# Optimization experiments

Hardware: AMD Instinct MI355X
Metric: run time of the kernel (lower is better)

The kernel has to match this reference:

```python
import jax, jax.numpy as jnp
import numpy as np

N_NODES = 100000
N_GRAPHS = 512
HID = 128
IN_DIM = 128
OUT_DIM = 10
N_EDGES = 1600000


def gcn_conv(x, src, dst, W, b, n):
    # PyG GCNConv: add self-loops, symmetric normalization D^-1/2 (A+I) D^-1/2, then linear.
    h = x @ W  # [N, H]
    deg = jnp.zeros((n,), h.dtype).at[dst].add(1.0) + 1.0  # +1 self-loop
    dinv = jax.lax.rsqrt(deg)
    norm = dinv[src] * dinv[dst]  # [E]
    agg = jnp.zeros_like(h).at[dst].add(h[src] * norm[:, None])
    agg = agg + h * (dinv * dinv)[:, None]  # self-loop messages
    return agg + b


def setup_inputs() -> dict:
    key = jax.random.key(0)
    ks = jax.random.split(key, 12)
    x = jax.random.normal(ks[0], (N_NODES, IN_DIM), jnp.float32)
    edge_index = jax.random.randint(ks[1], (2, N_EDGES), 0, N_NODES)
    batch = jnp.sort(jax.random.randint(ks[2], (N_NODES,), 0, N_GRAPHS))
    def lin(k, fan_in, shape):
        bound = 1.0 / np.sqrt(fan_in)
        return jax.random.uniform(k, shape, jnp.float32, -bound, bound)
    W1 = lin(ks[3], IN_DIM, (IN_DIM, HID)); b1 = lin(ks[4], IN_DIM, (HID,))
    W2 = lin(ks[5], HID, (HID, HID)); b2 = lin(ks[6], HID, (HID,))
    W3 = lin(ks[7], HID, (HID, HID)); b3 = lin(ks[8], HID, (HID,))
    Wc1 = lin(ks[9], 2 * HID, (2 * HID, HID)); bc1 = lin(ks[9], 2 * HID, (HID,))
    Wc2 = lin(ks[10], HID, (HID, OUT_DIM)); bc2 = lin(ks[11], HID, (OUT_DIM,))
    return {"x": x, "edge_index": edge_index, "batch": batch,
            "W1": W1, "b1": b1, "W2": W2, "b2": b2, "W3": W3, "b3": b3,
            "Wc1": Wc1, "bc1": bc1, "Wc2": Wc2, "bc2": bc2}


def reference(x, edge_index, batch, W1, b1, W2, b2, W3, b3, Wc1, bc1, Wc2, bc2):
    src, dst = edge_index[0], edge_index[1]
    n = x.shape[0]
    h = jax.nn.relu(gcn_conv(x, src, dst, W1, b1, n))
    h = jax.nn.relu(gcn_conv(h, src, dst, W2, b2, n))
    h = gcn_conv(h, src, dst, W3, b3, n)  # no relu after last conv
    # global mean pool
    sums = jax.ops.segment_sum(h, batch, num_segments=N_GRAPHS)
    cnt = jax.ops.segment_sum(jnp.ones((n,), h.dtype), batch, num_segments=N_GRAPHS)
    mean = sums / jnp.maximum(cnt, 1.0)[:, None]
    # global max pool
    mx = jax.ops.segment_max(h, batch, num_segments=N_GRAPHS)
    mx = jnp.where(jnp.isfinite(mx), mx, 0.0)
    g = jnp.concatenate([mean, mx], axis=1)  # [G, 2H]
    g = jax.nn.relu(g @ Wc1 + bc1)
    return g @ Wc2 + bc2
```

## Files before the change

### kernel.cpp

```cpp
#include <hip/hip_runtime.h>

#define H 128
#define CAP 64

typedef __attribute__((ext_vector_type(8))) short bf16x8;
typedef __attribute__((ext_vector_type(4))) float f32x4;

__device__ __forceinline__ unsigned short f2bf(float f) {
  unsigned u = __float_as_uint(f);
  unsigned r = u + 0x7FFFu + ((u >> 16) & 1u);
  return (unsigned short)(r >> 16);
}
__device__ __forceinline__ float bf2f(unsigned short s) {
  return __uint_as_float(((unsigned)s) << 16);
}

__global__ __launch_bounds__(256) void setup_all(
    const float* __restrict__ x,
    const float* __restrict__ W1, const float* __restrict__ W2, const float* __restrict__ W3,
    unsigned short* __restrict__ Xb, unsigned short* __restrict__ Wt,
    int* __restrict__ csr_src, int cap4,
    unsigned short* __restrict__ P, unsigned short* __restrict__ Q,
    int* __restrict__ cursor, int cur4,
    int n, int totalX4) {
  long long i = (long long)blockIdx.x * 256 + threadIdx.x;
  if (i < totalX4) {
    float4 v = *(const float4*)(x + i * 4);
    ushort4 o;
    o.x = f2bf(v.x); o.y = f2bf(v.y); o.z = f2bf(v.z); o.w = f2bf(v.w);
    *(ushort4*)(Xb + i * 4) = o;
    return;
  }
  i -= totalX4;
  if (i < cap4) {
    *(int4*)(csr_src + i * 4) = make_int4(n, n, n, n);
    return;
  }
  i -= cap4;
  if (i < 3 * H * H) {
    int w = (int)(i >> 14);
    int rem = (int)i & (H * H - 1);
    int c = rem >> 7;
    int k = rem & 127;
    const float* W = (w == 0) ? W1 : (w == 1) ? W2 : W3;
    Wt[i] = f2bf(W[(size_t)k * H + c]);
    return;
  }
  i -= 3 * H * H;
  if (i < cur4) {
    *(int4*)(cursor + i * 4) = make_int4(0, 0, 0, 0);
    return;
  }
  i -= cur4;
  if (i < H) {
    P[(size_t)n * H + i] = 0;
    Q[(size_t)n * H + i] = 0;
  }
}

__global__ __launch_bounds__(256) void csr_fill_fixed(
    const int* __restrict__ src, const int* __restrict__ dst,
    int* __restrict__ cursor, int* __restrict__ csr_src,
    int ne, int range, int slices) {
  int r = blockIdx.x & 7;
  int slice = blockIdx.x >> 3;
  int ne4 = ne / 4;
  int chunk4 = (ne4 + slices - 1) / slices;
  int beg4 = slice * chunk4;
  int end4 = beg4 + chunk4; if (end4 > ne4) end4 = ne4;
  int lo = r * range;
  int hi = lo + range;
  for (int e4 = beg4 + threadIdx.x; e4 < end4; e4 += 256) {
    int e = e4 * 4;
    int4 d = *(const int4*)(dst + e);
    if (d.x >= lo && d.x < hi) { int p = atomicAdd(&cursor[d.x], 1); if (p < CAP) csr_src[(size_t)d.x * CAP + p] = src[e + 0]; }
    if (d.y >= lo && d.y < hi) { int p = atomicAdd(&cursor[d.y], 1); if (p < CAP) csr_src[(size_t)d.y * CAP + p] = src[e + 1]; }
    if (d.z >= lo && d.z < hi) { int p = atomicAdd(&cursor[d.z], 1); if (p < CAP) csr_src[(size_t)d.z * CAP + p] = src[e + 2]; }
    if (d.w >= lo && d.w < hi) { int p = atomicAdd(&cursor[d.w], 1); if (p < CAP) csr_src[(size_t)d.w * CAP + p] = src[e + 3]; }
  }
  if (r == 0 && slice == 0) {
    int base = ne4 * 4;
    int t = base + threadIdx.x;
    if (t < ne) {
      int d = dst[t];
      int p = atomicAdd(&cursor[d], 1);
      if (p < CAP) csr_src[(size_t)d * CAP + p] = src[t];
    }
  }
}

__global__ void dinv_gstart(const int* __restrict__ deg, float* __restrict__ dinv,
                            const int* __restrict__ batch, int* __restrict__ g_start,
                            int n, int G) {
  int i = blockIdx.x * blockDim.x + threadIdx.x;
  if (i >= n) return;
  dinv[i] = rsqrtf((float)(deg[i] + 1));
  int b = batch[i];
  int prev = (i == 0) ? -1 : batch[i - 1];
  for (int g = prev + 1; g <= b; ++g) g_start[g] = i;
  if (i == n - 1) {
    for (int g = b + 1; g <= G; ++g) g_start[g] = n;
  }
}

#define SWLD 136
__global__ __launch_bounds__(256) void gemm_mfma(
    const unsigned short* __restrict__ Ab, const unsigned short* __restrict__ Wt,
    const float* __restrict__ dinv, unsigned short* __restrict__ outb, int n) {
  __shared__ unsigned short sW[H * SWLD];
  int tid = threadIdx.x;
  {
    int c = tid >> 1, hh = tid & 1;
    const int4* s = (const int4*)(Wt + (size_t)c * H + hh * 64);
    int4* d = (int4*)(sW + (size_t)c * SWLD + hh * 64);
#pragma unroll
    for (int i = 0; i < 8; ++i) d[i] = s[i];
  }
  __syncthreads();

  int wave = tid >> 6;
  int lane = tid & 63;
  int m = lane & 15;
  int quad = lane >> 4;
  int row = blockIdx.x * 64 + wave * 16 + m;
  bool rv = row < n;

  f32x4 acc[8];
#pragma unroll
  for (int t = 0; t < 8; ++t) acc[t] = (f32x4){0.f, 0.f, 0.f, 0.f};

  const unsigned short* arow = Ab + (size_t)(rv ? row : 0) * H;
#pragma unroll
  for (int k0 = 0; k0 < H; k0 += 32) {
    bf16x8 af;
    if (rv) af = *(const bf16x8*)(arow + k0 + quad * 8);
    else    af = (bf16x8){0, 0, 0, 0, 0, 0, 0, 0};
#pragma unroll
    for (int ct = 0; ct < 8; ++ct) {
      bf16x8 bfr = *(const bf16x8*)(sW + (size_t)(ct * 16 + m) * SWLD + k0 + quad * 8);
      acc[ct] = __builtin_amdgcn_mfma_f32_16x16x32_bf16(af, bfr, acc[ct], 0, 0, 0);
    }
  }

  int orow0 = blockIdx.x * 64 + wave * 16 + quad * 4;
#pragma unroll
  for (int r = 0; r < 4; ++r) {
    int orow = orow0 + r;
    if (orow < n) {
      float dv = dinv[orow];
      unsigned short* o = outb + (size_t)orow * H + m;
#pragma unroll
      for (int ct = 0; ct < 8; ++ct) o[ct * 16] = f2bf(acc[ct][r] * dv);
    }
  }
}

template <bool RELU, bool OUTF32>
__global__ __launch_bounds__(256) void aggregate_bf(
    const unsigned short* __restrict__ hs, const int* __restrict__ deg,
    const int* __restrict__ csr_src, const float* __restrict__ dinv,
    const float* __restrict__ b, void* __restrict__ outv, int n) {
  int node = blockIdx.x * 8 + (threadIdx.x >> 5);
  if (node >= n) return;
  int c = (threadIdx.x & 31) << 2;
  int beg = node * CAP;
  int end = beg + ((deg[node] + 7) & ~7);

  ushort4 sv = *(const ushort4*)(hs + (size_t)node * H + c);
  float4 acc;
  acc.x = bf2f(sv.x); acc.y = bf2f(sv.y); acc.z = bf2f(sv.z); acc.w = bf2f(sv.w);

  int4 ia, ib;
  if (beg < end) {
    ia = *(const int4*)(csr_src + beg);
    ib = *(const int4*)(csr_src + beg + 4);
  }
  for (int k = beg; k < end; k += 8) {
    int4 ca = ia, cb = ib;
    int kn = k + 8;
    if (kn < end) {
      ia = *(const int4*)(csr_src + kn);
      ib = *(const int4*)(csr_src + kn + 4);
    }
    ushort4 v0 = *(const ushort4*)(hs + (size_t)ca.x * H + c);
    ushort4 v1 = *(const ushort4*)(hs + (size_t)ca.y * H + c);
    ushort4 v2 = *(const ushort4*)(hs + (size_t)ca.z * H + c);
    ushort4 v3 = *(const ushort4*)(hs + (size_t)ca.w * H + c);
    ushort4 v4 = *(const ushort4*)(hs + (size_t)cb.x * H + c);
    ushort4 v5 = *(const ushort4*)(hs + (size_t)cb.y * H + c);
    ushort4 v6 = *(const ushort4*)(hs + (size_t)cb.z * H + c);
    ushort4 v7 = *(const ushort4*)(hs + (size_t)cb.w * H + c);
    acc.x += ((bf2f(v0.x) + bf2f(v1.x)) + (bf2f(v2.x) + bf2f(v3.x))) +
             ((bf2f(v4.x) + bf2f(v5.x)) + (bf2f(v6.x) + bf2f(v7.x)));
    acc.y += ((bf2f(v0.y) + bf2f(v1.y)) + (bf2f(v2.y) + bf2f(v3.y))) +
             ((bf2f(v4.y) + bf2f(v5.y)) + (bf2f(v6.y) + bf2f(v7.y)));
    acc.z += ((bf2f(v0.z) + bf2f(v1.z)) + (bf2f(v2.z) + bf2f(v3.z))) +
             ((bf2f(v4.z) + bf2f(v5.z)) + (bf2f(v6.z) + bf2f(v7.z)));
    acc.w += ((bf2f(v0.w) + bf2f(v1.w)) + (bf2f(v2.w) + bf2f(v3.w))) +
             ((bf2f(v4.w) + bf2f(v5.w)) + (bf2f(v6.w) + bf2f(v7.w)));
  }

  float dv = dinv[node];
  float4 bb = *(const float4*)(b + c);
  float4 o;
  o.x = fmaf(acc.x, dv, bb.x);
  o.y = fmaf(acc.y, dv, bb.y);
  o.z = fmaf(acc.z, dv, bb.z);
  o.w = fmaf(acc.w, dv, bb.w);
  if (RELU) {
    o.x = fmaxf(o.x, 0.f); o.y = fmaxf(o.y, 0.f);
    o.z = fmaxf(o.z, 0.f); o.w = fmaxf(o.w, 0.f);
  }
  if (OUTF32) {
    *(float4*)((float*)outv + (size_t)node * H + c) = o;
  } else {
    ushort4 ob;
    ob.x = f2bf(o.x); ob.y = f2bf(o.y); ob.z = f2bf(o.z); ob.w = f2bf(o.w);
    *(ushort4*)((unsigned short*)outv + (size_t)node * H + c) = ob;
  }
}

__global__ __launch_bounds__(256) void pool2(
    const float* __restrict__ h, const int* __restrict__ g_start,
    float* __restrict__ gmean, float* __restrict__ gmax, int n) {
  __shared__ float ssum[16][64];
  __shared__ float smax[16][64];
  int g = blockIdx.x >> 1;
  int half = blockIdx.x & 1;
  int beg = g_start[g];
  int end = g_start[g + 1];
  int q = threadIdx.x >> 4;
  int c = (threadIdx.x & 15) << 2;
  int cg = half * 64 + c;

  float4 s = make_float4(0.f, 0.f, 0.f, 0.f);
  float4 m = make_float4(-INFINITY, -INFINITY, -INFINITY, -INFINITY);
  for (int node = beg + q; node < end; node += 16) {
    float4 v = *(const float4*)(h + (size_t)node * H + cg);
    s.x += v.x; s.y += v.y; s.z += v.z; s.w += v.w;
    m.x = fmaxf(m.x, v.x); m.y = fmaxf(m.y, v.y);
    m.z = fmaxf(m.z, v.z); m.w = fmaxf(m.w, v.w);
  }
  *(float4*)&ssum[q][c] = s;
  *(float4*)&smax[q][c] = m;
  __syncthreads();

  int cnt = end - beg;
  int t = threadIdx.x;
  if (t < 64) {
    float tot = 0.f;
#pragma unroll
    for (int qq = 0; qq < 16; ++qq) tot += ssum[qq][t];
    gmean[(size_t)g * H + half * 64 + t] = tot / fmaxf((float)cnt, 1.0f);
  } else if (t < 128) {
    int cc = t - 64;
    float mx = -INFINITY;
#pragma unroll
    for (int qq = 0; qq < 16; ++qq) mx = fmaxf(mx, smax[qq][cc]);
    gmax[(size_t)g * H + half * 64 + cc] = (cnt == 0) ? 0.0f : mx;
  }
}

__global__ __launch_bounds__(128) void classify_kernel(
    const float* __restrict__ gmean, const float* __restrict__ gmax,
    const float* __restrict__ Wc1, const float* __restrict__ bc1,
    const float* __restrict__ Wc2, const float* __restrict__ bc2,
    float* __restrict__ out) {
  __shared__ float gv[2 * H];
  __shared__ float hid[H];
  int gid = blockIdx.x;
  int t = threadIdx.x;
  gv[t] = gmean[(size_t)gid * H + t];
  gv[H + t] = gmax[(size_t)gid * H + t];
  __syncthreads();
  float acc = 0.f;
#pragma unroll 8
  for (int k = 0; k < 2 * H; ++k) acc = fmaf(gv[k], Wc1[(size_t)k * H + t], acc);
  hid[t] = fmaxf(acc + bc1[t], 0.f);
  __syncthreads();
  if (t < 10) {
    float a2 = 0.f;
    for (int j = 0; j < H; ++j) a2 = fmaf(hid[j], Wc2[(size_t)j * 10 + t], a2);
    out[(size_t)gid * 10 + t] = a2 + bc2[t];
  }
}

extern "C" void kernel_launch(void* const* d_in, const int* in_sizes, int n_in,
                              void* d_out, int out_size, void* d_ws, size_t ws_size,
                              hipStream_t stream) {
  const float* x    = (const float*)d_in[0];
  const int* ei     = (const int*)d_in[1];
  const int* batch  = (const int*)d_in[2];
  const float* W1   = (const float*)d_in[3];
  const float* b1   = (const float*)d_in[4];
  const float* W2   = (const float*)d_in[5];
  const float* b2   = (const float*)d_in[6];
  const float* W3   = (const float*)d_in[7];
  const float* b3   = (const float*)d_in[8];
  const float* Wc1  = (const float*)d_in[9];
  const float* bc1  = (const float*)d_in[10];
  const float* Wc2  = (const float*)d_in[11];
  const float* bc2  = (const float*)d_in[12];
  float* out = (float*)d_out;

  const int n  = in_sizes[2];
  const int ne = in_sizes[1] / 2;
  const int G  = 512;
  const size_t NFb = (size_t)(n + 1) * H;

  const int* src = ei;
  const int* dst = ei + ne;

  unsigned short* P_bf = (unsigned short*)d_ws;
  unsigned short* Q_bf = P_bf + NFb;
  float*          F2f  = (float*)(Q_bf + NFb);
  unsigned short* Xb   = (unsigned short*)F2f;
  int* csr_src = (int*)(F2f + (size_t)n * H);
  const size_t csr_cap = (size_t)n * CAP;
  char* p = (char*)(csr_src + csr_cap);
  int*            cursor   = (int*)p;            p += (size_t)n * 4;
  float*          dinv     = (float*)p;          p += (size_t)n * 4;
  int*            g_start  = (int*)p;            p += (size_t)(G + 1) * 4;
  float*          gmean    = (float*)p;          p += (size_t)G * H * 4;
  float*          gmax     = (float*)p;          p += (size_t)G * H * 4;
  p = (char*)(((uintptr_t)p + 255) & ~(uintptr_t)255);
  unsigned short* Wt       = (unsigned short*)p; p += (size_t)3 * H * H * 2;

  {
    int totalX4 = n * H / 4;
    int cap4 = (int)(csr_cap / 4);
    int cur4 = n / 4;
    long long tot = (long long)totalX4 + cap4 + 3 * H * H + cur4 + H;
    int blocks = (int)((tot + 255) / 256);
    setup_all<<<blocks, 256, 0, stream>>>(x, W1, W2, W3, Xb, Wt, csr_src, cap4,
                                          P_bf, Q_bf, cursor, cur4, n, totalX4);
  }

  int range = (n + 7) / 8;
  csr_fill_fixed<<<128 * 8, 256, 0, stream>>>(src, dst, cursor, csr_src, ne, range, 128);
  dinv_gstart<<<(n + 255) / 256, 256, 0, stream>>>(cursor, dinv, batch, g_start, n, G);

  const int tile_grid = (n + 63) / 64;
  const int node_grid = (n + 7) / 8;

  gemm_mfma<<<tile_grid, 256, 0, stream>>>(Xb, Wt, dinv, Q_bf, n);
  aggregate_bf<true, false><<<node_grid, 256, 0, stream>>>(Q_bf, cursor, csr_src, dinv, b1, P_bf, n);

  gemm_mfma<<<tile_grid, 256, 0, stream>>>(P_bf, Wt + H * H, dinv, Q_bf, n);
  aggregate_bf<true, false><<<node_grid, 256, 0, stream>>>(Q_bf, cursor, csr_src, dinv, b2, P_bf, n);

  gemm_mfma<<<tile_grid, 256, 0, stream>>>(P_bf, Wt + 2 * H * H, dinv, Q_bf, n);
  aggregate_bf<false, true><<<node_grid, 256, 0, stream>>>(Q_bf, cursor, csr_src, dinv, b3, F2f, n);

  pool2<<<2 * G, 256, 0, stream>>>(F2f, g_start, gmean, gmax, n);
  classify_kernel<<<G, 128, 0, stream>>>(gmean, gmax, Wc1, bc1, Wc2, bc2, out);
}
```

Baseline: 460.7 us.

## Drop CSR sentinel padding fill and handle degree remainder with scalar tail loop

```diff
diff --git a/kernel.cpp b/kernel.cpp
--- a/kernel.cpp
+++ b/kernel.cpp
@@ -19,8 +19,6 @@
     const float* __restrict__ x,
     const float* __restrict__ W1, const float* __restrict__ W2, const float* __restrict__ W3,
     unsigned short* __restrict__ Xb, unsigned short* __restrict__ Wt,
-    int* __restrict__ csr_src, int cap4,
-    unsigned short* __restrict__ P, unsigned short* __restrict__ Q,
     int* __restrict__ cursor, int cur4,
     int n, int totalX4) {
   long long i = (long long)blockIdx.x * 256 + threadIdx.x;
@@ -32,11 +30,6 @@
     return;
   }
   i -= totalX4;
-  if (i < cap4) {
-    *(int4*)(csr_src + i * 4) = make_int4(n, n, n, n);
-    return;
-  }
-  i -= cap4;
   if (i < 3 * H * H) {
     int w = (int)(i >> 14);
     int rem = (int)i & (H * H - 1);
@@ -49,12 +42,6 @@
   i -= 3 * H * H;
   if (i < cur4) {
     *(int4*)(cursor + i * 4) = make_int4(0, 0, 0, 0);
-    return;
-  }
-  i -= cur4;
-  if (i < H) {
-    P[(size_t)n * H + i] = 0;
-    Q[(size_t)n * H + i] = 0;
   }
 }
 
@@ -163,25 +150,18 @@
   int node = blockIdx.x * 8 + (threadIdx.x >> 5);
   if (node >= n) return;
   int c = (threadIdx.x & 31) << 2;
-  int beg = node * CAP;
-  int end = beg + ((deg[node] + 7) & ~7);
+  int dg = deg[node];
+  int beg  = node * CAP;
+  int end8 = beg + (dg & ~7);
+  int end  = beg + dg;
 
   ushort4 sv = *(const ushort4*)(hs + (size_t)node * H + c);
   float4 acc;
   acc.x = bf2f(sv.x); acc.y = bf2f(sv.y); acc.z = bf2f(sv.z); acc.w = bf2f(sv.w);
 
-  int4 ia, ib;
-  if (beg < end) {
-    ia = *(const int4*)(csr_src + beg);
-    ib = *(const int4*)(csr_src + beg + 4);
-  }
-  for (int k = beg; k < end; k += 8) {
-    int4 ca = ia, cb = ib;
-    int kn = k + 8;
-    if (kn < end) {
-      ia = *(const int4*)(csr_src + kn);
-      ib = *(const int4*)(csr_src + kn + 4);
-    }
+  for (int k = beg; k < end8; k += 8) {
+    int4 ca = *(const int4*)(csr_src + k);
+    int4 cb = *(const int4*)(csr_src + k + 4);
     ushort4 v0 = *(const ushort4*)(hs + (size_t)ca.x * H + c);
     ushort4 v1 = *(const ushort4*)(hs + (size_t)ca.y * H + c);
     ushort4 v2 = *(const ushort4*)(hs + (size_t)ca.z * H + c);
@@ -198,6 +178,12 @@
              ((bf2f(v4.z) + bf2f(v5.z)) + (bf2f(v6.z) + bf2f(v7.z)));
     acc.w += ((bf2f(v0.w) + bf2f(v1.w)) + (bf2f(v2.w) + bf2f(v3.w))) +
              ((bf2f(v4.w) + bf2f(v5.w)) + (bf2f(v6.w) + bf2f(v7.w)));
+  }
+  for (int k = end8; k < end; ++k) {
+    int s = csr_src[k];
+    ushort4 v = *(const ushort4*)(hs + (size_t)s * H + c);
+    acc.x += bf2f(v.x); acc.y += bf2f(v.y);
+    acc.z += bf2f(v.z); acc.w += bf2f(v.w);
   }
 
   float dv = dinv[node];
@@ -306,7 +292,7 @@
   const int n  = in_sizes[2];
   const int ne = in_sizes[1] / 2;
   const int G  = 512;
-  const size_t NFb = (size_t)(n + 1) * H;
+  const size_t NFb = (size_t)n * H;
 
   const int* src = ei;
   const int* dst = ei + ne;
@@ -315,7 +301,7 @@
   unsigned short* Q_bf = P_bf + NFb;
   float*          F2f  = (float*)(Q_bf + NFb);
   unsigned short* Xb   = (unsigned short*)F2f;
-  int* csr_src = (int*)(F2f + (size_t)n * H);
+  int* csr_src = (int*)(F2f + NFb);
   const size_t csr_cap = (size_t)n * CAP;
   char* p = (char*)(csr_src + csr_cap);
   int*            cursor   = (int*)p;            p += (size_t)n * 4;
@@ -328,16 +314,14 @@
 
   {
     int totalX4 = n * H / 4;
-    int cap4 = (int)(csr_cap / 4);
     int cur4 = n / 4;
-    long long tot = (long long)totalX4 + cap4 + 3 * H * H + cur4 + H;
+    long long tot = (long long)totalX4 + 3 * H * H + cur4;
     int blocks = (int)((tot + 255) / 256);
-    setup_all<<<blocks, 256, 0, stream>>>(x, W1, W2, W3, Xb, Wt, csr_src, cap4,
-                                          P_bf, Q_bf, cursor, cur4, n, totalX4);
+    setup_all<<<blocks, 256, 0, stream>>>(x, W1, W2, W3, Xb, Wt, cursor, cur4, n, totalX4);
   }
 
   int range = (n + 7) / 8;
-  csr_fill_fixed<<<128 * 8, 256, 0, stream>>>(src, dst, cursor, csr_src, ne, range, 128);
+  csr_fill_fixed<<<256 * 8, 256, 0, stream>>>(src, dst, cursor, csr_src, ne, range, 256);
   dinv_gstart<<<(n + 255) / 256, 256, 0, stream>>>(cursor, dinv, batch, g_start, n, G);
 
   const int tile_grid = (n + 63) / 64;
```

After: 471.2 us. +2.3%, slower.
